# Optimization experiments

Hardware: AMD Instinct MI355X
Metric: run time of the kernel (lower is better)

## Reference

```python
import jax, jax.numpy as jnp
import numpy as np

B, S, H, NH = 1, 2048, 2048, 32
HD = H // NH  # 64
DFF = 4 * H
EPS = 1e-5


def layer_norm(x, w, b):
    mu = jnp.mean(x, axis=-1, keepdims=True)
    var = jnp.var(x, axis=-1, keepdims=True)
    return (x - mu) * jax.lax.rsqrt(var + EPS) * w + b


def setup_inputs() -> dict:
    key = jax.random.key(0)
    ks = jax.random.split(key, 16)
    std = 0.02
    hidden_states = jax.random.normal(ks[0], (B, S, H), dtype=jnp.float32)
    # additive causal mask [1,1,S,S]
    causal = jnp.tril(jnp.ones((S, S), dtype=jnp.bool_))
    attention_mask = jnp.where(causal, 0.0, -1e9).astype(jnp.float32)[None, None]
    p = lambda k, shp: (jax.random.normal(k, shp, dtype=jnp.float32) * std)
    return {
        "hidden_states": hidden_states,
        "attention_mask": attention_mask,
        "ln1_w": jnp.ones((H,), jnp.float32), "ln1_b": jnp.zeros((H,), jnp.float32),
        "wq": p(ks[1], (H, H)), "bq": jnp.zeros((H,), jnp.float32),
        "wk": p(ks[2], (H, H)), "bk": jnp.zeros((H,), jnp.float32),
        "wv": p(ks[3], (H, H)), "bv": jnp.zeros((H,), jnp.float32),
        "wo": p(ks[4], (H, H)), "bo": jnp.zeros((H,), jnp.float32),
        "w1": p(ks[5], (H, DFF)), "b1": jnp.zeros((DFF,), jnp.float32),
        "w2": p(ks[6], (DFF, H)), "b2": jnp.zeros((H,), jnp.float32),
        "ln2_w": jnp.ones((H,), jnp.float32), "ln2_b": jnp.zeros((H,), jnp.float32),
    }


def reference(hidden_states, attention_mask, ln1_w, ln1_b, wq, bq, wk, bk, wv, bv,
              wo, bo, w1, b1, w2, b2, ln2_w, ln2_b):
    x = hidden_states
    # --- pre-norm attention ---
    residual = x
    h = layer_norm(x, ln1_w, ln1_b)
    scaling = HD ** -0.5
    q = (h @ wq + bq).reshape(B, S, NH, HD) * scaling
    k = (h @ wk + bk).reshape(B, S, NH, HD)
    v = (h @ wv + bv).reshape(B, S, NH, HD)
    scores = jnp.einsum('bqhd,bkhd->bhqk', q, k) + attention_mask
    p = jax.nn.softmax(scores, axis=-1)  # dropout is identity in eval
    attn = jnp.einsum('bhqk,bkhd->bqhd', p, v).reshape(B, S, H)
    attn = attn @ wo + bo
    x = residual + attn
    # --- pre-norm MLP ---
    residual = x
    h = layer_norm(x, ln2_w, ln2_b)
    h = jax.nn.gelu(h @ w1 + b1, approximate=False) @ w2 + b2
    return residual + h
```

## Files before the change

### kernel.cpp

```cpp
#include <hip/hip_runtime.h>
#include <math.h>

#define H 2048
#define S 2048
#define NH 32
#define HD 64
#define DFF 8192

typedef __attribute__((ext_vector_type(4))) float f32x4;
typedef __attribute__((ext_vector_type(8))) short short8;
typedef __attribute__((ext_vector_type(4))) short s16x4;

static __device__ __forceinline__ ushort f2bf(float f) {
  unsigned u = __float_as_uint(f);
  u += 0x7fff + ((u >> 16) & 1);
  return (ushort)(u >> 16);
}

static __device__ __forceinline__ float bf2f(ushort u) {
  return __uint_as_float(((unsigned)u) << 16);
}

static __device__ __forceinline__ void gl_lds16(const ushort* g, ushort* l) {
  __builtin_amdgcn_global_load_lds(
      (__attribute__((address_space(1))) const void*)g,
      (__attribute__((address_space(3))) void*)l, 16, 0, 0);
}

__global__ __launch_bounds__(256) void transpose_all_kernel(
    const float* __restrict__ wq, const float* __restrict__ wk,
    const float* __restrict__ wv, const float* __restrict__ wo,
    const float* __restrict__ w1, const float* __restrict__ w2,
    ushort* __restrict__ oQKV, ushort* __restrict__ oO,
    ushort* __restrict__ o1, ushort* __restrict__ o2) {
  __shared__ __align__(16) ushort tile[64][72];
  int id = blockIdx.x;
  const float* W;
  ushort* Wt;
  int K, N, bx, by;
  if (id < 4096) {
    int which = id >> 10, r = id & 1023;
    bx = r & 31; by = r >> 5; K = H; N = H;
    W = (which == 0) ? wq : (which == 1) ? wk : (which == 2) ? wv : wo;
    Wt = (which == 3) ? oO : oQKV + (size_t)which * H * H;
  } else if (id < 8192) {
    int r = id - 4096;
    bx = r & 127; by = r >> 7; K = H; N = DFF;
    W = w1; Wt = o1;
  } else {
    int r = id - 8192;
    bx = r & 31; by = r >> 5; K = DFF; N = H;
    W = w2; Wt = o2;
  }
  int n0 = bx * 64, k0 = by * 64;
  int t = threadIdx.x;
  int lk = t >> 4;
  int ln4 = (t & 15) * 4;
#pragma unroll
  for (int p = 0; p < 4; p++) {
    int k = p * 16 + lk;
    float4 v = *reinterpret_cast<const float4*>(&W[(size_t)(k0 + k) * N + n0 + ln4]);
    float vv[4] = {v.x, v.y, v.z, v.w};
#pragma unroll
    for (int i = 0; i < 4; i++) {
      int row = ln4 + i;
      int slot = ((k >> 3) ^ (row & 7));
      tile[row][(slot << 3) + (k & 7)] = f2bf(vv[i]);
    }
  }
  __syncthreads();
  int n = t >> 2;
  int kq = (t & 3) * 8;
#pragma unroll
  for (int p = 0; p < 2; p++) {
    int kk = kq + p * 32;
    int slot = ((kk >> 3) ^ (n & 7));
    short8 o = *reinterpret_cast<const short8*>(&tile[n][slot << 3]);
    *reinterpret_cast<short8*>(&Wt[(size_t)(n0 + n) * K + k0 + kk]) = o;
  }
}

__global__ __launch_bounds__(256) void ln_kernel(
    const float* __restrict__ x, const float* __restrict__ w,
    const float* __restrict__ b, ushort* __restrict__ out) {
  int row = blockIdx.x, t = threadIdx.x;
  const float4* xr = reinterpret_cast<const float4*>(x + (size_t)row * H);
  float4 v0 = xr[t * 2], v1 = xr[t * 2 + 1];
  float s = v0.x + v0.y + v0.z + v0.w + v1.x + v1.y + v1.z + v1.w;
  float q = v0.x * v0.x + v0.y * v0.y + v0.z * v0.z + v0.w * v0.w +
            v1.x * v1.x + v1.y * v1.y + v1.z * v1.z + v1.w * v1.w;
#pragma unroll
  for (int off = 32; off > 0; off >>= 1) {
    s += __shfl_down(s, off, 64);
    q += __shfl_down(q, off, 64);
  }
  __shared__ float sm[8];
  int lane = t & 63, wv = t >> 6;
  if (lane == 0) { sm[wv] = s; sm[wv + 4] = q; }
  __syncthreads();
  s = sm[0] + sm[1] + sm[2] + sm[3];
  q = sm[4] + sm[5] + sm[6] + sm[7];
  float mu = s * (1.0f / H);
  float var = q * (1.0f / H) - mu * mu;
  float rs = rsqrtf(var + 1e-5f);
  const float4* wr = reinterpret_cast<const float4*>(w);
  const float4* br = reinterpret_cast<const float4*>(b);
  float4 w0 = wr[t * 2], w1v = wr[t * 2 + 1], b0 = br[t * 2], b1v = br[t * 2 + 1];
  short8 pk;
  pk[0] = (short)f2bf((v0.x - mu) * rs * w0.x + b0.x);
  pk[1] = (short)f2bf((v0.y - mu) * rs * w0.y + b0.y);
  pk[2] = (short)f2bf((v0.z - mu) * rs * w0.z + b0.z);
  pk[3] = (short)f2bf((v0.w - mu) * rs * w0.w + b0.w);
  pk[4] = (short)f2bf((v1.x - mu) * rs * w1v.x + b1v.x);
  pk[5] = (short)f2bf((v1.y - mu) * rs * w1v.y + b1v.y);
  pk[6] = (short)f2bf((v1.z - mu) * rs * w1v.z + b1v.z);
  pk[7] = (short)f2bf((v1.w - mu) * rs * w1v.w + b1v.w);
  *reinterpret_cast<short8*>(out + (size_t)row * H + t * 8) = pk;
}

__global__ __launch_bounds__(256) void combine2_kernel(
    const float* __restrict__ res, const ushort* __restrict__ p0,
    const ushort* __restrict__ p1, const float* __restrict__ bias,
    float* __restrict__ out) {
  size_t i = (size_t)blockIdx.x * 256 + threadIdx.x;
  float4 a0 = reinterpret_cast<const float4*>(res)[i * 2];
  float4 a1 = reinterpret_cast<const float4*>(res)[i * 2 + 1];
  short8 c = reinterpret_cast<const short8*>(p0)[i];
  short8 d = reinterpret_cast<const short8*>(p1)[i];
  int col = (int)((i * 8) & (H - 1));
  float4 b0 = *reinterpret_cast<const float4*>(bias + col);
  float4 b1 = *reinterpret_cast<const float4*>(bias + col + 4);
  float4 o0, o1;
  o0.x = a0.x + bf2f((ushort)c[0]) + bf2f((ushort)d[0]) + b0.x;
  o0.y = a0.y + bf2f((ushort)c[1]) + bf2f((ushort)d[1]) + b0.y;
  o0.z = a0.z + bf2f((ushort)c[2]) + bf2f((ushort)d[2]) + b0.z;
  o0.w = a0.w + bf2f((ushort)c[3]) + bf2f((ushort)d[3]) + b0.w;
  o1.x = a1.x + bf2f((ushort)c[4]) + bf2f((ushort)d[4]) + b1.x;
  o1.y = a1.y + bf2f((ushort)c[5]) + bf2f((ushort)d[5]) + b1.y;
  o1.z = a1.z + bf2f((ushort)c[6]) + bf2f((ushort)d[6]) + b1.z;
  o1.w = a1.w + bf2f((ushort)c[7]) + bf2f((ushort)d[7]) + b1.w;
  reinterpret_cast<float4*>(out)[i * 2] = o0;
  reinterpret_cast<float4*>(out)[i * 2 + 1] = o1;
}

__global__ __launch_bounds__(256) void combine_ln_kernel(
    const float* __restrict__ res, const ushort* __restrict__ p0,
    const ushort* __restrict__ p1, const float* __restrict__ bias,
    const float* __restrict__ lw, const float* __restrict__ lb,
    float* __restrict__ xout, ushort* __restrict__ lnout) {
  int row = blockIdx.x, t = threadIdx.x;
  const float4* rr = reinterpret_cast<const float4*>(res + (size_t)row * H);
  short8 c = *reinterpret_cast<const short8*>(p0 + (size_t)row * H + t * 8);
  short8 d = *reinterpret_cast<const short8*>(p1 + (size_t)row * H + t * 8);
  const float4* bb = reinterpret_cast<const float4*>(bias);
  float4 a0 = rr[t * 2], a1 = rr[t * 2 + 1];
  float4 e0 = bb[t * 2], e1 = bb[t * 2 + 1];
  float4 v0, v1;
  v0.x = a0.x + bf2f((ushort)c[0]) + bf2f((ushort)d[0]) + e0.x;
  v0.y = a0.y + bf2f((ushort)c[1]) + bf2f((ushort)d[1]) + e0.y;
  v0.z = a0.z + bf2f((ushort)c[2]) + bf2f((ushort)d[2]) + e0.z;
  v0.w = a0.w + bf2f((ushort)c[3]) + bf2f((ushort)d[3]) + e0.w;
  v1.x = a1.x + bf2f((ushort)c[4]) + bf2f((ushort)d[4]) + e1.x;
  v1.y = a1.y + bf2f((ushort)c[5]) + bf2f((ushort)d[5]) + e1.y;
  v1.z = a1.z + bf2f((ushort)c[6]) + bf2f((ushort)d[6]) + e1.z;
  v1.w = a1.w + bf2f((ushort)c[7]) + bf2f((ushort)d[7]) + e1.w;
  float4* xo = reinterpret_cast<float4*>(xout + (size_t)row * H);
  xo[t * 2] = v0;
  xo[t * 2 + 1] = v1;
  float s = v0.x + v0.y + v0.z + v0.w + v1.x + v1.y + v1.z + v1.w;
  float q = v0.x * v0.x + v0.y * v0.y + v0.z * v0.z + v0.w * v0.w +
            v1.x * v1.x + v1.y * v1.y + v1.z * v1.z + v1.w * v1.w;
#pragma unroll
  for (int off = 32; off > 0; off >>= 1) {
    s += __shfl_down(s, off, 64);
    q += __shfl_down(q, off, 64);
  }
  __shared__ float sm[8];
  int lane = t & 63, wv = t >> 6;
  if (lane == 0) { sm[wv] = s; sm[wv + 4] = q; }
  __syncthreads();
  s = sm[0] + sm[1] + sm[2] + sm[3];
  q = sm[4] + sm[5] + sm[6] + sm[7];
  float mu = s * (1.0f / H);
  float var = q * (1.0f / H) - mu * mu;
  float rs = rsqrtf(var + 1e-5f);
  const float4* wr = reinterpret_cast<const float4*>(lw);
  const float4* br = reinterpret_cast<const float4*>(lb);
  float4 w0 = wr[t * 2], w1v = wr[t * 2 + 1], b0 = br[t * 2], b1v = br[t * 2 + 1];
  short8 pk;
  pk[0] = (short)f2bf((v0.x - mu) * rs * w0.x + b0.x);
  pk[1] = (short)f2bf((v0.y - mu) * rs * w0.y + b0.y);
  pk[2] = (short)f2bf((v0.z - mu) * rs * w0.z + b0.z);
  pk[3] = (short)f2bf((v0.w - mu) * rs * w0.w + b0.w);
  pk[4] = (short)f2bf((v1.x - mu) * rs * w1v.x + b1v.x);
  pk[5] = (short)f2bf((v1.y - mu) * rs * w1v.y + b1v.y);
  pk[6] = (short)f2bf((v1.z - mu) * rs * w1v.z + b1v.z);
  pk[7] = (short)f2bf((v1.w - mu) * rs * w1v.w + b1v.w);
  *reinterpret_cast<short8*>(lnout + (size_t)row * H + t * 8) = pk;
}

template <int MODE, int NI>
__global__ __launch_bounds__(512, 2) void gemm256_kernel(
    const ushort* __restrict__ A, const ushort* __restrict__ Bt,
    const float* __restrict__ bias, const float* __restrict__ biasB,
    const float* __restrict__ biasC,
    ushort* __restrict__ outb, ushort* __restrict__ outbV,
    int M, int N, int lda, int kbeg, int klen) {
  constexpr int BN = NI * 64;
  __shared__ __align__(16) ushort As[2][256 * 64];
  __shared__ __align__(16) ushort Bs[2][BN * 64];
  int tid = threadIdx.x, lane = tid & 63, w = tid >> 6;
  int lm = lane & 15, kg = lane >> 4;
  int wr = w >> 2, wc = w & 3;
  int gx = gridDim.x, nwg = gx * gridDim.y;
  int orig = blockIdx.y * gx + blockIdx.x;
  int wg = (orig & 7) * (nwg >> 3) + (orig >> 3);
  int m0 = (wg % gx) * 256, n0 = (wg / gx) * BN;
  int kb0 = kbeg + blockIdx.z * klen;

  f32x4 acc[8][NI] = {};

  const ushort* srcA[4];
  const ushort* srcB[NI];
  int dbase[4];
#pragma unroll
  for (int q = 0; q < 4; q++) {
    int g = q * 512 + tid;
    int row = g >> 3, gc = g & 7;
    int col = (gc ^ (row & 7)) << 3;
    srcA[q] = A + (size_t)(m0 + row) * lda + kb0 + col;
    if (q < NI) srcB[q] = Bt + (size_t)(n0 + row) * lda + kb0 + col;
    dbase[q] = (q * 512 + w * 64) * 8;
  }

  const ushort* aB0 = &As[0][(wr * 128 + lm) * 64 + ((kg ^ (lm & 7)) << 3)];
  const ushort* aB1 = &As[0][(wr * 128 + lm) * 64 + (((4 + kg) ^ (lm & 7)) << 3)];
  const ushort* bB0 = &Bs[0][(wc * 16 * NI + lm) * 64 + ((kg ^ (lm & 7)) << 3)];
  const ushort* bB1 = &Bs[0][(wc * 16 * NI + lm) * 64 + (((4 + kg) ^ (lm & 7)) << 3)];

  int nK = klen >> 6;
#pragma unroll
  for (int q = 0; q < NI; q++) gl_lds16(srcB[q], &Bs[0][dbase[q]]);
  gl_lds16(srcA[0], &As[0][dbase[0]]);
  gl_lds16(srcA[2], &As[0][dbase[2]]);
  gl_lds16(srcA[1], &As[0][dbase[1]]);
  gl_lds16(srcA[3], &As[0][dbase[3]]);
  asm volatile("s_waitcnt vmcnt(2)" ::: "memory");
  __builtin_amdgcn_s_barrier();

  for (int kt = 0; kt < nK; kt++) {
    int cur = kt & 1, nxt = cur ^ 1;
    bool hn = (kt + 1 < nK);
    int ko = (kt + 1) << 6;
    const ushort* a0 = aB0 + cur * 16384;
    const ushort* a1 = aB1 + cur * 16384;
    const ushort* b0 = bB0 + cur * (BN * 64);
    const ushort* b1 = bB1 + cur * (BN * 64);

    short8 af[4][2], bfr[NI][2];

#pragma unroll
    for (int i = 0; i < 4; i++) {
      af[i][0] = *reinterpret_cast<const short8*>(a0 + i * 1024);
      af[i][1] = *reinterpret_cast<const short8*>(a1 + i * 1024);
    }
#pragma unroll
    for (int n = 0; n < NI; n++) {
      bfr[n][0] = *reinterpret_cast<const short8*>(b0 + n * 1024);
      bfr[n][1] = *reinterpret_cast<const short8*>(b1 + n * 1024);
    }
    if (hn) {
#pragma unroll
      for (int q = 0; q < NI; q++) gl_lds16(srcB[q] + ko, &Bs[nxt][dbase[q]]);
    }
    __builtin_amdgcn_s_barrier();
    __builtin_amdgcn_s_setprio(1);
#pragma unroll
    for (int i = 0; i < 4; i++)
#pragma unroll
      for (int n = 0; n < NI; n++)
#pragma unroll
        for (int s = 0; s < 2; s++)
          acc[i][n] = __builtin_amdgcn_mfma_f32_16x16x32_bf16(af[i][s], bfr[n][s], acc[i][n], 0, 0, 0);
    __builtin_amdgcn_s_setprio(0);
    if (hn) {
      if constexpr (NI == 4) asm volatile("s_waitcnt vmcnt(4)" ::: "memory");
      else if constexpr (NI == 3) asm volatile("s_waitcnt vmcnt(3)" ::: "memory");
      else asm volatile("s_waitcnt vmcnt(2)" ::: "memory");
    } else {
      asm volatile("s_waitcnt vmcnt(0)" ::: "memory");
    }
    __builtin_amdgcn_s_barrier();

#pragma unroll
    for (int i = 0; i < 4; i++) {
      af[i][0] = *reinterpret_cast<const short8*>(a0 + 4096 + i * 1024);
      af[i][1] = *reinterpret_cast<const short8*>(a1 + 4096 + i * 1024);
    }
    if (hn) {
      gl_lds16(srcA[0] + ko, &As[nxt][dbase[0]]);
      gl_lds16(srcA[2] + ko, &As[nxt][dbase[2]]);
      gl_lds16(srcA[1] + ko, &As[nxt][dbase[1]]);
      gl_lds16(srcA[3] + ko, &As[nxt][dbase[3]]);
    }
    __builtin_amdgcn_s_barrier();
    __builtin_amdgcn_s_setprio(1);
#pragma unroll
    for (int i = 0; i < 4; i++)
#pragma unroll
      for (int n = 0; n < NI; n++)
#pragma unroll
        for (int s = 0; s < 2; s++)
          acc[4 + i][n] = __builtin_amdgcn_mfma_f32_16x16x32_bf16(af[i][s], bfr[n][s], acc[4 + i][n], 0, 0, 0);
    __builtin_amdgcn_s_setprio(0);
    if (hn) asm volatile("s_waitcnt vmcnt(2)" ::: "memory");
    __builtin_amdgcn_s_barrier();
  }

#pragma unroll
  for (int mi = 0; mi < 8; mi++) {
#pragma unroll
    for (int ni = 0; ni < NI; ni++) {
      int row0 = m0 + wr * 128 + mi * 16 + kg * 4;
      int col = n0 + wc * 16 * NI + ni * 16 + lm;
      f32x4 v4 = acc[mi][ni];
      if (MODE == 0) {
        if (col < 2 * H) {
          float bb = (col < H) ? bias[col] : biasB[col - H];
          float sc = (col < H) ? 0.125f : 1.0f;
          size_t base = (size_t)(col >> 11) * ((size_t)S * H) + (col & (H - 1));
#pragma unroll
          for (int r = 0; r < 4; r++)
            outb[base + (size_t)(row0 + r) * H] = f2bf((v4[r] + bb) * sc);
        } else {
          float bb = biasC[col - 2 * H];
          s16x4 pk;
#pragma unroll
          for (int r = 0; r < 4; r++) pk[r] = (short)f2bf(v4[r] + bb);
          *reinterpret_cast<s16x4*>(outbV + (size_t)(col - 2 * H) * S + row0) = pk;
        }
      } else if (MODE == 1) {
#pragma unroll
        for (int r = 0; r < 4; r++) {
          float t = v4[r] + bias[col];
          outb[(size_t)(row0 + r) * N + col] = f2bf(0.5f * t * (1.0f + erff(t * 0.70710678118f)));
        }
      } else {
#pragma unroll
        for (int r = 0; r < 4; r++)
          outb[(size_t)blockIdx.z * M * N + (size_t)(row0 + r) * N + col] = f2bf(v4[r]);
      }
    }
  }
}

__global__ __launch_bounds__(512) void attn_kernel(
    const ushort* __restrict__ Q, const ushort* __restrict__ Kmat,
    const ushort* __restrict__ VT, ushort* __restrict__ ctx) {
  __shared__ __align__(16) ushort Ks[2][128 * 64];
  __shared__ __align__(16) ushort Vs[2][64 * 128];
  __shared__ __align__(16) ushort Ps[8 * 16 * 64];
  int h = blockIdx.x;
  int x = blockIdx.y;
  int tid = threadIdx.x, lane = tid & 63, w = tid >> 6;
  int lm = lane & 15, kg = lane >> 4;

  int qbA = x, qbB = 15 - x;
  int tA = x + 1;
  const int nt = 17;

  short8 qa[2];
#pragma unroll
  for (int ks = 0; ks < 2; ks++)
    qa[ks] = *reinterpret_cast<const short8*>(
        Q + (size_t)(qbA * 128 + w * 16 + lm) * H + h * 64 + ks * 32 + kg * 8);

  float m_run[4], l_run[4];
  f32x4 o_acc[4] = {};
#pragma unroll
  for (int r = 0; r < 4; r++) { m_run[r] = -1e30f; l_run[r] = 0.f; }

  auto stage = [&](int kb, int buf) {
#pragma unroll
    for (int p = 0; p < 2; p++) {
      int gbase = p * 512 + w * 64;
      int gran = gbase + lane;
      int krow = gran >> 3, gk = gran & 7;
      gl_lds16(Kmat + (size_t)(kb * 128 + krow) * H + h * 64 + ((gk ^ (krow & 7)) << 3),
               &Ks[buf][gbase * 8]);
    }
#pragma unroll
    for (int p = 0; p < 2; p++) {
      int gbase = p * 512 + w * 64;
      int gran = gbase + lane;
      int vrow = gran >> 4, gv = gran & 15;
      gl_lds16(VT + (size_t)(h * 64 + vrow) * S + kb * 128 + ((gv ^ (vrow & 15)) << 3),
               &Vs[buf][gbase * 8]);
    }
  };

  stage(0, 0);
  __syncthreads();

  for (int t = 0; t < nt; t++) {
    int cur = t & 1;
    if (t + 1 < nt) {
      int tn = t + 1;
      stage((tn < tA) ? tn : tn - tA, cur ^ 1);
    }
    bool diag = (t == tA - 1) || (t == nt - 1);

    f32x4 sacc[8] = {};
#pragma unroll
    for (int j = 0; j < 8; j++) {
      int krow = j * 16 + lm;
#pragma unroll
      for (int ks = 0; ks < 2; ks++) {
        short8 kf = *reinterpret_cast<const short8*>(
            &Ks[cur][krow * 64 + (((ks * 4 + kg) ^ (lm & 7)) << 3)]);
        sacc[j] = __builtin_amdgcn_mfma_f32_16x16x32_bf16(qa[ks], kf, sacc[j], 0, 0, 0);
      }
    }
    if (diag) {
#pragma unroll
      for (int j = 0; j < 8; j++)
#pragma unroll
        for (int r = 0; r < 4; r++)
          if (j * 16 + lm > w * 16 + kg * 4 + r) sacc[j][r] = -1e30f;
    }

#pragma unroll
    for (int r = 0; r < 4; r++) {
      float mx = sacc[0][r];
#pragma unroll
      for (int j = 1; j < 8; j++) mx = fmaxf(mx, sacc[j][r]);
      mx = fmaxf(mx, __shfl_xor(mx, 1, 64));
      mx = fmaxf(mx, __shfl_xor(mx, 2, 64));
      mx = fmaxf(mx, __shfl_xor(mx, 4, 64));
      mx = fmaxf(mx, __shfl_xor(mx, 8, 64));
      float mnew = fmaxf(m_run[r], mx);
      float sc = __expf(m_run[r] - mnew);
      m_run[r] = mnew;
      float ps = 0.f;
#pragma unroll
      for (int j = 0; j < 8; j++) {
        float p = __expf(sacc[j][r] - mnew);
        sacc[j][r] = p;
        ps += p;
      }
      ps += __shfl_xor(ps, 1, 64);
      ps += __shfl_xor(ps, 2, 64);
      ps += __shfl_xor(ps, 4, 64);
      ps += __shfl_xor(ps, 8, 64);
      l_run[r] = l_run[r] * sc + ps;
#pragma unroll
      for (int jd = 0; jd < 4; jd++) o_acc[jd][r] *= sc;
    }

#pragma unroll
    for (int c = 0; c < 2; c++) {
#pragma unroll
      for (int jj = 0; jj < 4; jj++)
#pragma unroll
        for (int r = 0; r < 4; r++) {
          int rl = kg * 4 + r;
          int col = jj * 16 + lm;
          Ps[w * 1024 + rl * 64 + (((col >> 3) ^ (rl & 7)) << 3) + (col & 7)] =
              f2bf(sacc[c * 4 + jj][r]);
        }
      short8 pa[2];
#pragma unroll
      for (int ks = 0; ks < 2; ks++)
        pa[ks] = *reinterpret_cast<const short8*>(
            &Ps[w * 1024 + lm * 64 + (((ks * 4 + kg) ^ (lm & 7)) << 3)]);
#pragma unroll
      for (int jd = 0; jd < 4; jd++) {
        int d = jd * 16 + lm;
#pragma unroll
        for (int ks = 0; ks < 2; ks++) {
          short8 vf = *reinterpret_cast<const short8*>(
              &Vs[cur][d * 128 + (((c * 8 + ks * 4 + kg) ^ lm) << 3)]);
          o_acc[jd] = __builtin_amdgcn_mfma_f32_16x16x32_bf16(pa[ks], vf, o_acc[jd], 0, 0, 0);
        }
      }
    }

    if (t == tA - 1) {
#pragma unroll
      for (int jd = 0; jd < 4; jd++)
#pragma unroll
        for (int r = 0; r < 4; r++)
          ctx[(size_t)(qbA * 128 + w * 16 + kg * 4 + r) * H + h * 64 + jd * 16 + lm] =
              f2bf(o_acc[jd][r] / l_run[r]);
#pragma unroll
      for (int r = 0; r < 4; r++) { m_run[r] = -1e30f; l_run[r] = 0.f; }
#pragma unroll
      for (int jd = 0; jd < 4; jd++) o_acc[jd] = f32x4{0.f, 0.f, 0.f, 0.f};
#pragma unroll
      for (int ks = 0; ks < 2; ks++)
        qa[ks] = *reinterpret_cast<const short8*>(
            Q + (size_t)(qbB * 128 + w * 16 + lm) * H + h * 64 + ks * 32 + kg * 8);
    }
    __syncthreads();
  }

#pragma unroll
  for (int jd = 0; jd < 4; jd++)
#pragma unroll
    for (int r = 0; r < 4; r++)
      ctx[(size_t)(qbB * 128 + w * 16 + kg * 4 + r) * H + h * 64 + jd * 16 + lm] =
          f2bf(o_acc[jd][r] / l_run[r]);
}

extern "C" void kernel_launch(void* const* d_in, const int* in_sizes, int n_in,
                              void* d_out, int out_size, void* d_ws, size_t ws_size,
                              hipStream_t stream) {
  const float* x = (const float*)d_in[0];
  const float* ln1w = (const float*)d_in[2];
  const float* ln1b = (const float*)d_in[3];
  const float* wq = (const float*)d_in[4];
  const float* bq = (const float*)d_in[5];
  const float* wk = (const float*)d_in[6];
  const float* bk = (const float*)d_in[7];
  const float* wv = (const float*)d_in[8];
  const float* bv = (const float*)d_in[9];
  const float* wo = (const float*)d_in[10];
  const float* bo = (const float*)d_in[11];
  const float* w1 = (const float*)d_in[12];
  const float* b1 = (const float*)d_in[13];
  const float* w2 = (const float*)d_in[14];
  const float* b2 = (const float*)d_in[15];
  const float* ln2w = (const float*)d_in[16];
  const float* ln2b = (const float*)d_in[17];
  float* out = (float*)d_out;

  char* ws = (char*)d_ws;
  const size_t MB = 1024 * 1024;
  const size_t SH = (size_t)S * H;
  ushort* WT_QKV = (ushort*)(ws);
  ushort* WT_O = (ushort*)(ws + 24 * MB);
  ushort* WT_1 = (ushort*)(ws + 32 * MB);
  ushort* WT_2 = (ushort*)(ws + 64 * MB);
  ushort* LNO = (ushort*)(ws + 96 * MB);
  ushort* QKVB = (ushort*)(ws + 104 * MB);
  ushort* VTb = (ushort*)(ws + 128 * MB);
  ushort* CTX = (ushort*)(ws + 136 * MB);
  float* X1 = (float*)(ws + 144 * MB);
  ushort* MID = (ushort*)(ws);
  ushort* SPA = (ushort*)(ws + 104 * MB);
  ushort* SPM = (ushort*)(ws + 32 * MB);

  transpose_all_kernel<<<12288, 256, 0, stream>>>(
      wq, wk, wv, wo, w1, w2, WT_QKV, WT_O, WT_1, WT_2);

  ln_kernel<<<S, 256, 0, stream>>>(x, ln1w, ln1b, LNO);

  gemm256_kernel<0, 3><<<dim3(S / 256, 3 * H / 192), 512, 0, stream>>>(
      LNO, WT_QKV, bq, bk, bv, QKVB, VTb, S, 3 * H, H, 0, H);

  attn_kernel<<<dim3(NH, 8), 512, 0, stream>>>(QKVB, QKVB + SH, VTb, CTX);

  gemm256_kernel<3, 2><<<dim3(S / 256, H / 128, 2), 512, 0, stream>>>(
      CTX, WT_O, nullptr, nullptr, nullptr, SPA, nullptr, S, H, H, 0, H / 2);
  combine_ln_kernel<<<S, 256, 0, stream>>>(x, SPA, SPA + SH, bo, ln2w, ln2b, X1, LNO);

  gemm256_kernel<1, 4><<<dim3(S / 256, DFF / 256), 512, 0, stream>>>(
      LNO, WT_1, b1, nullptr, nullptr, MID, nullptr, S, DFF, H, 0, H);

  gemm256_kernel<3, 2><<<dim3(S / 256, H / 128, 2), 512, 0, stream>>>(
      MID, WT_2, nullptr, nullptr, nullptr, SPM, nullptr, S, H, DFF, 0, DFF / 2);
  combine2_kernel<<<SH / 2048, 256, 0, stream>>>(X1, SPM, SPM + SH, b2, out);
}
```

Baseline: 370.1 us.

## Replace pipelined 256-row GEMM with simple single-buffered 128x128 tile GEMM

Swaps the double-buffered 256xBN GEMM, which used 512 threads, prefetch overlap and setprio, for a 128x128 tile kernel with 256 threads, K-step 32 and one LDS buffer synchronised by two __syncthreads per step. All four GEMM launches move to the new kernel with grids adjusted to match. This gives smaller tiles, more workgroups and higher occupancy per CU, at the cost of losing global-to-LDS prefetch overlap, lowering arithmetic intensity per tile and adding more barriers.

```diff
diff --git a/kernel.cpp b/kernel.cpp
--- a/kernel.cpp
+++ b/kernel.cpp
@@ -199,131 +199,72 @@
   *reinterpret_cast<short8*>(lnout + (size_t)row * H + t * 8) = pk;
 }
 
-template <int MODE, int NI>
-__global__ __launch_bounds__(512, 2) void gemm256_kernel(
+template <int MODE>
+__global__ __launch_bounds__(256, 4) void gemm128_kernel(
     const ushort* __restrict__ A, const ushort* __restrict__ Bt,
     const float* __restrict__ bias, const float* __restrict__ biasB,
     const float* __restrict__ biasC,
     ushort* __restrict__ outb, ushort* __restrict__ outbV,
     int M, int N, int lda, int kbeg, int klen) {
-  constexpr int BN = NI * 64;
-  __shared__ __align__(16) ushort As[2][256 * 64];
-  __shared__ __align__(16) ushort Bs[2][BN * 64];
+  __shared__ __align__(16) ushort As[128 * 32];
+  __shared__ __align__(16) ushort Bs[128 * 32];
   int tid = threadIdx.x, lane = tid & 63, w = tid >> 6;
   int lm = lane & 15, kg = lane >> 4;
-  int wr = w >> 2, wc = w & 3;
+  int wm = (w >> 1) * 64, wn = (w & 1) * 64;
   int gx = gridDim.x, nwg = gx * gridDim.y;
   int orig = blockIdx.y * gx + blockIdx.x;
   int wg = (orig & 7) * (nwg >> 3) + (orig >> 3);
-  int m0 = (wg % gx) * 256, n0 = (wg / gx) * BN;
+  int m0 = (wg % gx) * 128, n0 = (wg / gx) * 128;
   int kb0 = kbeg + blockIdx.z * klen;
 
-  f32x4 acc[8][NI] = {};
-
-  const ushort* srcA[4];
-  const ushort* srcB[NI];
-  int dbase[4];
-#pragma unroll
-  for (int q = 0; q < 4; q++) {
-    int g = q * 512 + tid;
-    int row = g >> 3, gc = g & 7;
-    int col = (gc ^ (row & 7)) << 3;
+  f32x4 acc[4][4] = {};
+
+  const ushort* srcA[2];
+  const ushort* srcB[2];
+  int dbase[2];
+#pragma unroll
+  for (int q = 0; q < 2; q++) {
+    int g = q * 256 + tid;
+    int row = g >> 2, gc = g & 3;
+    int col = (gc ^ (row & 3)) << 3;
     srcA[q] = A + (size_t)(m0 + row) * lda + kb0 + col;
-    if (q < NI) srcB[q] = Bt + (size_t)(n0 + row) * lda + kb0 + col;
-    dbase[q] = (q * 512 + w * 64) * 8;
-  }
-
-  const ushort* aB0 = &As[0][(wr * 128 + lm) * 64 + ((kg ^ (lm & 7)) << 3)];
-  const ushort* aB1 = &As[0][(wr * 128 + lm) * 64 + (((4 + kg) ^ (lm & 7)) << 3)];
-  const ushort* bB0 = &Bs[0][(wc * 16 * NI + lm) * 64 + ((kg ^ (lm & 7)) << 3)];
-  const ushort* bB1 = &Bs[0][(wc * 16 * NI + lm) * 64 + (((4 + kg) ^ (lm & 7)) << 3)];
-
-  int nK = klen >> 6;
-#pragma unroll
-  for (int q = 0; q < NI; q++) gl_lds16(srcB[q], &Bs[0][dbase[q]]);
-  gl_lds16(srcA[0], &As[0][dbase[0]]);
-  gl_lds16(srcA[2], &As[0][dbase[2]]);
-  gl_lds16(srcA[1], &As[0][dbase[1]]);
-  gl_lds16(srcA[3], &As[0][dbase[3]]);
-  asm volatile("s_waitcnt vmcnt(2)" ::: "memory");
-  __builtin_amdgcn_s_barrier();
-
+    srcB[q] = Bt + (size_t)(n0 + row) * lda + kb0 + col;
+    dbase[q] = (q * 256 + w * 64) * 8;
+  }
+
+  const ushort* aR = &As[(wm + lm) * 32 + ((kg ^ (lm & 3)) << 3)];
+  const ushort* bR = &Bs[(wn + lm) * 32 + ((kg ^ (lm & 3)) << 3)];
+
+  int nK = klen >> 5;
   for (int kt = 0; kt < nK; kt++) {
-    int cur = kt & 1, nxt = cur ^ 1;
-    bool hn = (kt + 1 < nK);
-    int ko = (kt + 1) << 6;
-    const ushort* a0 = aB0 + cur * 16384;
-    const ushort* a1 = aB1 + cur * 16384;
-    const ushort* b0 = bB0 + cur * (BN * 64);
-    const ushort* b1 = bB1 + cur * (BN * 64);
-
-    short8 af[4][2], bfr[NI][2];
-
-#pragma unroll
-    for (int i = 0; i < 4; i++) {
-      af[i][0] = *reinterpret_cast<const short8*>(a0 + i * 1024);
-      af[i][1] = *reinterpret_cast<const short8*>(a1 + i * 1024);
-    }
-#pragma unroll
-    for (int n = 0; n < NI; n++) {
-      bfr[n][0] = *reinterpret_cast<const short8*>(b0 + n * 1024);
-      bfr[n][1] = *reinterpret_cast<const short8*>(b1 + n * 1024);
-    }
-    if (hn) {
-#pragma unroll
-      for (int q = 0; q < NI; q++) gl_lds16(srcB[q] + ko, &Bs[nxt][dbase[q]]);
-    }
-    __builtin_amdgcn_s_barrier();
-    __builtin_amdgcn_s_setprio(1);
+    int ko = kt << 5;
+    __syncthreads();
+    gl_lds16(srcA[0] + ko, As + dbase[0]);
+    gl_lds16(srcA[1] + ko, As + dbase[1]);
+    gl_lds16(srcB[0] + ko, Bs + dbase[0]);
+    gl_lds16(srcB[1] + ko, Bs + dbase[1]);
+    __syncthreads();
+    short8 af[4], bfr[4];
 #pragma unroll
     for (int i = 0; i < 4; i++)
-#pragma unroll
-      for (int n = 0; n < NI; n++)
-#pragma unroll
-        for (int s = 0; s < 2; s++)
-          acc[i][n] = __builtin_amdgcn_mfma_f32_16x16x32_bf16(af[i][s], bfr[n][s], acc[i][n], 0, 0, 0);
-    __builtin_amdgcn_s_setprio(0);
-    if (hn) {
-      if constexpr (NI == 4) asm volatile("s_waitcnt vmcnt(4)" ::: "memory");
-      else if constexpr (NI == 3) asm volatile("s_waitcnt vmcnt(3)" ::: "memory");
-      else asm volatile("s_waitcnt vmcnt(2)" ::: "memory");
-    } else {
-      asm volatile("s_waitcnt vmcnt(0)" ::: "memory");
-    }
-    __builtin_amdgcn_s_barrier();
-
-#pragma unroll
-    for (int i = 0; i < 4; i++) {
-      af[i][0] = *reinterpret_cast<const short8*>(a0 + 4096 + i * 1024);
-      af[i][1] = *reinterpret_cast<const short8*>(a1 + 4096 + i * 1024);
-    }
-    if (hn) {
-      gl_lds16(srcA[0] + ko, &As[nxt][dbase[0]]);
-      gl_lds16(srcA[2] + ko, &As[nxt][dbase[2]]);
-      gl_lds16(srcA[1] + ko, &As[nxt][dbase[1]]);
-      gl_lds16(srcA[3] + ko, &As[nxt][dbase[3]]);
-    }
-    __builtin_amdgcn_s_barrier();
-    __builtin_amdgcn_s_setprio(1);
+      af[i] = *reinterpret_cast<const short8*>(aR + i * 512);
+#pragma unroll
+    for (int j = 0; j < 4; j++)
+      bfr[j] = *reinterpret_cast<const short8*>(bR + j * 512);
 #pragma unroll
     for (int i = 0; i < 4; i++)
 #pragma unroll
-      for (int n = 0; n < NI; n++)
-#pragma unroll
-        for (int s = 0; s < 2; s++)
-          acc[4 + i][n] = __builtin_amdgcn_mfma_f32_16x16x32_bf16(af[i][s], bfr[n][s], acc[4 + i][n], 0, 0, 0);
-    __builtin_amdgcn_s_setprio(0);
-    if (hn) asm volatile("s_waitcnt vmcnt(2)" ::: "memory");
-    __builtin_amdgcn_s_barrier();
-  }
-
-#pragma unroll
-  for (int mi = 0; mi < 8; mi++) {
-#pragma unroll
-    for (int ni = 0; ni < NI; ni++) {
-      int row0 = m0 + wr * 128 + mi * 16 + kg * 4;
-      int col = n0 + wc * 16 * NI + ni * 16 + lm;
-      f32x4 v4 = acc[mi][ni];
+      for (int j = 0; j < 4; j++)
+        acc[i][j] = __builtin_amdgcn_mfma_f32_16x16x32_bf16(af[i], bfr[j], acc[i][j], 0, 0, 0);
+  }
+
+#pragma unroll
+  for (int i = 0; i < 4; i++) {
+#pragma unroll
+    for (int j = 0; j < 4; j++) {
+      int row0 = m0 + wm + i * 16 + kg * 4;
+      int col = n0 + wn + j * 16 + lm;
+      f32x4 v4 = acc[i][j];
       if (MODE == 0) {
         if (col < 2 * H) {
           float bb = (col < H) ? bias[col] : biasB[col - H];
@@ -555,19 +496,19 @@
 
   ln_kernel<<<S, 256, 0, stream>>>(x, ln1w, ln1b, LNO);
 
-  gemm256_kernel<0, 3><<<dim3(S / 256, 3 * H / 192), 512, 0, stream>>>(
+  gemm128_kernel<0><<<dim3(S / 128, 3 * H / 128), 256, 0, stream>>>(
       LNO, WT_QKV, bq, bk, bv, QKVB, VTb, S, 3 * H, H, 0, H);
 
   attn_kernel<<<dim3(NH, 8), 512, 0, stream>>>(QKVB, QKVB + SH, VTb, CTX);
 
-  gemm256_kernel<3, 2><<<dim3(S / 256, H / 128, 2), 512, 0, stream>>>(
+  gemm128_kernel<3><<<dim3(S / 128, H / 128, 2), 256, 0, stream>>>(
       CTX, WT_O, nullptr, nullptr, nullptr, SPA, nullptr, S, H, H, 0, H / 2);
   combine_ln_kernel<<<S, 256, 0, stream>>>(x, SPA, SPA + SH, bo, ln2w, ln2b, X1, LNO);
 
-  gemm256_kernel<1, 4><<<dim3(S / 256, DFF / 256), 512, 0, stream>>>(
+  gemm128_kernel<1><<<dim3(S / 128, DFF / 128), 256, 0, stream>>>(
       LNO, WT_1, b1, nullptr, nullptr, MID, nullptr, S, DFF, H, 0, H);
 
-  gemm256_kernel<3, 2><<<dim3(S / 256, H / 128, 2), 512, 0, stream>>>(
+  gemm128_kernel<3><<<dim3(S / 128, H / 128, 2), 256, 0, stream>>>(
       MID, WT_2, nullptr, nullptr, nullptr, SPM, nullptr, S, H, DFF, 0, DFF / 2);
   combine2_kernel<<<SH / 2048, 256, 0, stream>>>(X1, SPM, SPM + SH, b2, out);
 }
```

After: 402.1 us. 1.09x slower.
